# Kernel optimization log

Measured on AMD Instinct MI355X. Metric: run time of the kernel, lower is better.

Reference implementation:

```python
import jax, jax.numpy as jnp
import numpy as np

B, T, D, H = 2, 2048, 1024, 16
DH = D // H

def setup_inputs() -> dict:
    key = jax.random.key(0)
    ks = jax.random.split(key, 5)
    scale = 1.0 / np.sqrt(D)
    x = jax.random.normal(ks[0], (B, T, D), dtype=jnp.float32)
    Wq = jax.random.normal(ks[1], (D, D), dtype=jnp.float32) * scale
    Wk = jax.random.normal(ks[2], (D, D), dtype=jnp.float32) * scale
    Wv = jax.random.normal(ks[3], (D, D), dtype=jnp.float32) * scale
    Wo = jax.random.normal(ks[4], (D, D), dtype=jnp.float32) * scale
    # causal mask: True means masked (matches torch masked_fill semantics)
    mask = jnp.triu(jnp.ones((T, T), dtype=bool), k=1)
    return {"x": x, "mask": mask, "Wq": Wq, "Wk": Wk, "Wv": Wv, "Wo": Wo}

def reference(x, mask, Wq, Wk, Wv, Wo):
    b, t, c = x.shape
    # projections -> [B, H, T, DH]
    def split_heads(y):
        return y.reshape(b, t, H, DH).transpose(0, 2, 1, 3)
    q = split_heads(x @ Wq)
    k = split_heads(x @ Wk)
    v = split_heads(x @ Wv)
    # scores [B, H, T, T]
    att = jnp.einsum('bhqd,bhkd->bhqk', q, k) / jnp.sqrt(jnp.float32(DH))
    att = jnp.where(mask, -jnp.inf, att)
    att = jax.nn.softmax(att, axis=-1)
    # dropout=0.0 (eval-mode determinism)
    out = jnp.einsum('bhqk,bhkd->bhqd', att, v)
    out = out.transpose(0, 2, 1, 3).reshape(b, t, c)
    return out @ Wo
```

## Files before the change

kernel.cpp:

```cpp
#include <hip/hip_runtime.h>
#include <stdint.h>

typedef unsigned short u16;
typedef unsigned int u32;
typedef __attribute__((ext_vector_type(8))) short s16x8;
typedef __attribute__((ext_vector_type(4))) float f32x4;
typedef __attribute__((ext_vector_type(8))) unsigned short u16x8;
typedef __attribute__((ext_vector_type(4))) unsigned short u16x4;

#define T_ 2048
#define D_ 1024
#define H_ 16
#define DH_ 64

#define QSCALE_LOG2E 0.18033688011112042f

#if __has_builtin(__builtin_amdgcn_exp2f)
#define EXP2(x) __builtin_amdgcn_exp2f(x)
#else
#define EXP2(x) exp2f(x)
#endif

__device__ __forceinline__ float bf2f(u16 u) {
    union { unsigned int i; float f; } x; x.i = ((unsigned int)u) << 16; return x.f;
}
__device__ __forceinline__ u16 f2bf(float f) {
    union { float f; unsigned int i; } x; x.f = f;
    unsigned int u = x.i;
    u += 0x7fffu + ((u >> 16) & 1u);
    return (u16)(u >> 16);
}
__device__ __forceinline__ u32 pack_rn(float a, float b) {
    union { float f; u32 u; } ua, ub; ua.f = a; ub.f = b;
    return ((ua.u + 0x8000u) >> 16) | ((ub.u + 0x8000u) & 0xffff0000u);
}

__device__ __forceinline__ void gload16(const u16* g, u16* l) {
    __builtin_amdgcn_global_load_lds(
        (const __attribute__((address_space(1))) void*)g,
        (__attribute__((address_space(3))) void*)l,
        16, 0, 0);
}

__global__ __launch_bounds__(256) void cvt_x_kernel(const float* __restrict__ x,
                                                    u16* __restrict__ xb) {
    int i = (blockIdx.x * 256 + threadIdx.x) * 4;
    float4 v = *(const float4*)(x + i);
    u16x4 o;
    o[0] = f2bf(v.x); o[1] = f2bf(v.y); o[2] = f2bf(v.z); o[3] = f2bf(v.w);
    *(u16x4*)(xb + i) = o;
}

__global__ __launch_bounds__(256) void transpose_w_kernel(const float* __restrict__ Wq,
                                                          const float* __restrict__ Wk,
                                                          const float* __restrict__ Wv,
                                                          const float* __restrict__ Wo,
                                                          u16* __restrict__ WT) {
    __shared__ float tile[32][33];
    int s = blockIdx.z;
    const float* W = (s == 0) ? Wq : (s == 1) ? Wk : (s == 2) ? Wv : Wo;
    int n0 = blockIdx.x * 32;
    int k0 = blockIdx.y * 32;
    int tx = threadIdx.x, ty = threadIdx.y;
    #pragma unroll
    for (int j = 0; j < 32; j += 8)
        tile[ty + j][tx] = W[(k0 + ty + j) * D_ + n0 + tx];
    __syncthreads();
    u16* dst = WT + (size_t)s * D_ * D_;
    #pragma unroll
    for (int j = 0; j < 32; j += 8)
        dst[(n0 + ty + j) * D_ + k0 + tx] = f2bf(tile[tx][ty + j]);
}

template <int MODE>
__global__ __launch_bounds__(256) void gemm_bt(const u16* __restrict__ A,
                                               const u16* __restrict__ Bt,
                                               u16* __restrict__ Qw,
                                               u16* __restrict__ Kw,
                                               u16* __restrict__ Vw,
                                               float* __restrict__ Cout) {
    __shared__ __align__(16) u16 As[2][128 * 32];
    __shared__ __align__(16) u16 Bs[2][128 * 32];
    const int m0 = blockIdx.x * 128, n0 = blockIdx.y * 128;
    int tid = threadIdx.x;
    int w = tid >> 6, lane = tid & 63, quad = lane >> 4, l15 = lane & 15;
    int wr = w >> 1, wc = w & 1;

    int nb0 = (w << 7), nb1 = nb0 + 64;
    int c0 = nb0 + lane, c1 = nb1 + lane;
    int r0 = c0 >> 2, k0off = (c0 & 3) << 3;
    int r1 = c1 >> 2, k1off = (c1 & 3) << 3;
    const u16* Ar0 = A + (size_t)(m0 + r0) * D_ + k0off;
    const u16* Ar1 = A + (size_t)(m0 + r1) * D_ + k1off;
    const u16* Br0 = Bt + (size_t)(n0 + r0) * D_ + k0off;
    const u16* Br1 = Bt + (size_t)(n0 + r1) * D_ + k1off;

    f32x4 acc[4][4];
    #pragma unroll
    for (int mi = 0; mi < 4; ++mi)
        #pragma unroll
        for (int ni = 0; ni < 4; ++ni) acc[mi][ni] = (f32x4){0.f, 0.f, 0.f, 0.f};

    gload16(Ar0, &As[0][nb0 << 3]);
    gload16(Ar1, &As[0][nb1 << 3]);
    gload16(Br0, &Bs[0][nb0 << 3]);
    gload16(Br1, &Bs[0][nb1 << 3]);

    for (int k0 = 0; k0 < D_; k0 += 32) {
        int buf = (k0 >> 5) & 1;
        __syncthreads();
        if (k0 + 32 < D_) {
            int kn = k0 + 32;
            gload16(Ar0 + kn, &As[buf ^ 1][nb0 << 3]);
            gload16(Ar1 + kn, &As[buf ^ 1][nb1 << 3]);
            gload16(Br0 + kn, &Bs[buf ^ 1][nb0 << 3]);
            gload16(Br1 + kn, &Bs[buf ^ 1][nb1 << 3]);
        }
        s16x8 af[4], bf[4];
        #pragma unroll
        for (int mi = 0; mi < 4; ++mi)
            af[mi] = *(const s16x8*)&As[buf][((wr * 64 + mi * 16 + l15) << 5) + (quad << 3)];
        #pragma unroll
        for (int ni = 0; ni < 4; ++ni)
            bf[ni] = *(const s16x8*)&Bs[buf][((wc * 64 + ni * 16 + l15) << 5) + (quad << 3)];
        #pragma unroll
        for (int mi = 0; mi < 4; ++mi)
            #pragma unroll
            for (int ni = 0; ni < 4; ++ni)
                acc[mi][ni] = __builtin_amdgcn_mfma_f32_16x16x32_bf16(af[mi], bf[ni],
                                                                      acc[mi][ni], 0, 0, 0);
    }

    #pragma unroll
    for (int mi = 0; mi < 4; ++mi) {
        int mbase = m0 + wr * 64 + mi * 16 + quad * 4;
        #pragma unroll
        for (int ni = 0; ni < 4; ++ni) {
            int n = n0 + wc * 64 + ni * 16 + l15;
            if (MODE == 0) {
                int b = mbase >> 11, t0 = mbase & 2047;
                int sel = n >> 10, nn = n & 1023;
                int h = nn >> 6, dh = nn & 63;
                int bhidx = (b << 4) + h;
                if (sel == 0) {
                    #pragma unroll
                    for (int r = 0; r < 4; ++r)
                        Qw[(size_t)(bhidx * T_ + t0 + r) * DH_ + dh] =
                            f2bf(acc[mi][ni][r] * QSCALE_LOG2E);
                } else if (sel == 1) {
                    #pragma unroll
                    for (int r = 0; r < 4; ++r)
                        Kw[(size_t)(bhidx * T_ + t0 + r) * DH_ + dh] = f2bf(acc[mi][ni][r]);
                } else {
                    uint2 pk;
                    pk.x = pack_rn(acc[mi][ni][0], acc[mi][ni][1]);
                    pk.y = pack_rn(acc[mi][ni][2], acc[mi][ni][3]);
                    *(uint2*)(Vw + ((size_t)bhidx * DH_ + dh) * T_ + t0) = pk;
                }
            } else {
                #pragma unroll
                for (int r = 0; r < 4; ++r)
                    Cout[(size_t)(mbase + r) * D_ + n] = acc[mi][ni][r];
            }
        }
    }
}

__global__ __launch_bounds__(256) void attn_mfma_kernel(const u16* __restrict__ Qg,
                                                        const u16* __restrict__ Kg,
                                                        const u16* __restrict__ Vt,
                                                        u16* __restrict__ att) {
    __shared__ __align__(16) u16 Kbuf[2][64 * 64];
    __shared__ __align__(16) u16 Vbuf[2][64 * 64];
    __shared__ __align__(16) u16 Ps[4][16][72];

    int bx = (int)gridDim.x - 1 - (int)blockIdx.x;
    int bh = blockIdx.y;
    int tid = threadIdx.x;
    int w = tid >> 6, lane = tid & 63, quad = lane >> 4, l15 = lane & 15;
    int q0 = bx * 64;
    int q0w = q0 + 16 * w;

    const u16* Qb = Qg + (size_t)bh * T_ * DH_;
    const u16* Kb = Kg + (size_t)bh * T_ * DH_;
    const u16* Vb = Vt + (size_t)bh * DH_ * T_;

    s16x8 qb0 = *(const s16x8*)(Qb + (size_t)(q0w + l15) * DH_ + quad * 8);
    s16x8 qb1 = *(const s16x8*)(Qb + (size_t)(q0w + l15) * DH_ + quad * 8 + 32);

    int nb0 = (w << 7);
    int nb1 = (w << 7) + 64;
    int n0c = nb0 + lane, n1c = nb1 + lane;
    int r0 = n0c >> 3, c0s = n0c & 7, g0 = (r0 << 3) + (c0s ^ (r0 & 7));
    int r1 = n1c >> 3, c1s = n1c & 7, g1 = (r1 << 3) + (c1s ^ (r1 & 7));

    gload16(Kb + (g0 << 3), &Kbuf[0][nb0 << 3]);
    gload16(Kb + (g1 << 3), &Kbuf[0][nb1 << 3]);
    gload16(Vb + (size_t)r0 * T_ + ((g0 & 7) << 3), &Vbuf[0][nb0 << 3]);
    gload16(Vb + (size_t)r1 * T_ + ((g1 & 7) << 3), &Vbuf[0][nb1 << 3]);

    f32x4 og[4] = {{0.f,0.f,0.f,0.f},{0.f,0.f,0.f,0.f},{0.f,0.f,0.f,0.f},{0.f,0.f,0.f,0.f}};
    float lpart = 0.f;

    for (int kt = 0; kt <= bx; ++kt) {
        int buf = kt & 1;
        __syncthreads();

        if (kt < bx) {
            int kb2 = (kt + 1) << 6;
            const u16* Ktile = Kb + (size_t)kb2 * DH_;
            gload16(Ktile + (g0 << 3), &Kbuf[buf ^ 1][nb0 << 3]);
            gload16(Ktile + (g1 << 3), &Kbuf[buf ^ 1][nb1 << 3]);
            gload16(Vb + (size_t)r0 * T_ + kb2 + ((g0 & 7) << 3), &Vbuf[buf ^ 1][nb0 << 3]);
            gload16(Vb + (size_t)r1 * T_ + kb2 + ((g1 & 7) << 3), &Vbuf[buf ^ 1][nb1 << 3]);
        }

        f32x4 st[4];
        #pragma unroll
        for (int g = 0; g < 4; ++g) {
            int r = (g << 4) + l15;
            int cc = quad ^ (r & 7);
            s16x8 ka0 = *(const s16x8*)&Kbuf[buf][((r << 3) + cc) << 3];
            s16x8 ka1 = *(const s16x8*)&Kbuf[buf][((r << 3) + (cc ^ 4)) << 3];
            f32x4 z = {0.f, 0.f, 0.f, 0.f};
            st[g] = __builtin_amdgcn_mfma_f32_16x16x32_bf16(ka0, qb0, z, 0, 0, 0);
            st[g] = __builtin_amdgcn_mfma_f32_16x16x32_bf16(ka1, qb1, st[g], 0, 0, 0);
        }

        if (kt == bx) {
            int rowq = (w << 4) + l15;
            #pragma unroll
            for (int g = 0; g < 4; ++g)
                #pragma unroll
                for (int r = 0; r < 4; ++r)
                    if ((g << 4) + (quad << 2) + r > rowq) st[g][r] = -INFINITY;
        }

        #pragma unroll
        for (int g = 0; g < 4; ++g)
            #pragma unroll
            for (int r = 0; r < 4; ++r) {
                float p = EXP2(st[g][r]);
                st[g][r] = p;
                lpart += p;
            }

        #pragma unroll
        for (int g = 0; g < 4; ++g) {
            uint2 pk;
            pk.x = pack_rn(st[g][0], st[g][1]);
            pk.y = pack_rn(st[g][2], st[g][3]);
            *(uint2*)&Ps[w][l15][g * 16 + quad * 4] = pk;
        }
        s16x8 pb0 = *(const s16x8*)&Ps[w][l15][quad * 8];
        s16x8 pb1 = *(const s16x8*)&Ps[w][l15][quad * 8 + 32];

        #pragma unroll
        for (int g = 0; g < 4; ++g) {
            int r = (g << 4) + l15;
            int cc = quad ^ (r & 7);
            s16x8 va0 = *(const s16x8*)&Vbuf[buf][((r << 3) + cc) << 3];
            s16x8 va1 = *(const s16x8*)&Vbuf[buf][((r << 3) + (cc ^ 4)) << 3];
            og[g] = __builtin_amdgcn_mfma_f32_16x16x32_bf16(va0, pb0, og[g], 0, 0, 0);
            og[g] = __builtin_amdgcn_mfma_f32_16x16x32_bf16(va1, pb1, og[g], 0, 0, 0);
        }
    }

    float l = lpart;
    l += __shfl_xor(l, 16);
    l += __shfl_xor(l, 32);
    float inv = 1.f / l;
    int b = bh >> 4, h = bh & 15;
    u16* dst = att + (size_t)(b * T_ + q0w + l15) * D_ + (h << 6);
    #pragma unroll
    for (int g = 0; g < 4; ++g) {
        uint2 pk;
        pk.x = (u32)f2bf(og[g][0] * inv) | ((u32)f2bf(og[g][1] * inv) << 16);
        pk.y = (u32)f2bf(og[g][2] * inv) | ((u32)f2bf(og[g][3] * inv) << 16);
        *(uint2*)(dst + (g << 4) + (quad << 2)) = pk;
    }
}

extern "C" void kernel_launch(void* const* d_in, const int* in_sizes, int n_in,
                              void* d_out, int out_size, void* d_ws, size_t ws_size,
                              hipStream_t stream) {
    const float* x  = (const float*)d_in[0];
    const float* Wq = (const float*)d_in[2];
    const float* Wk = (const float*)d_in[3];
    const float* Wv = (const float*)d_in[4];
    const float* Wo = (const float*)d_in[5];
    float* out = (float*)d_out;

    char* ws = (char*)d_ws;
    u16* xb  = (u16*)(ws);
    u16* WT  = (u16*)(ws + (8ull  << 20));
    u16* Qw  = (u16*)(ws + (16ull << 20));
    u16* Kw  = (u16*)(ws + (24ull << 20));
    u16* Vw  = (u16*)(ws + (32ull << 20));
    u16* att = (u16*)(ws + (40ull << 20));

    cvt_x_kernel<<<dim3(4096), dim3(256), 0, stream>>>(x, xb);
    transpose_w_kernel<<<dim3(32, 32, 4), dim3(32, 8), 0, stream>>>(Wq, Wk, Wv, Wo, WT);
    gemm_bt<0><<<dim3(32, 24), dim3(256), 0, stream>>>(xb, WT, Qw, Kw, Vw, nullptr);
    attn_mfma_kernel<<<dim3(32, 32), dim3(256), 0, stream>>>(Qw, Kw, Vw, att);
    gemm_bt<1><<<dim3(32, 8), dim3(256), 0, stream>>>(att, WT + 3ull * 1048576ull,
                                                      nullptr, nullptr, nullptr, out);
}
```

Baseline: 215.0 us.

## Process 128 query rows per attention block and narrow output GEMM tiles

The attention kernel now has each block handle two 64-row query tiles, so every K/V tile staged in LDS feeds twice as many MFMAs, and the grid halves to 16x32. Causal masking is adjusted for the two sub-tiles. The output projection gets its own kernel with 128x64 tiles, doubling its block count from 256 to 512 to improve CU occupancy. The trade-offs are more registers per attention thread and fewer, longer attention blocks, which could worsen load balance across the causal triangle.

```diff
diff --git a/kernel.cpp b/kernel.cpp
--- a/kernel.cpp
+++ b/kernel.cpp
@@ -72,13 +72,11 @@
         dst[(n0 + ty + j) * D_ + k0 + tx] = f2bf(tile[tx][ty + j]);
 }
 
-template <int MODE>
-__global__ __launch_bounds__(256) void gemm_bt(const u16* __restrict__ A,
-                                               const u16* __restrict__ Bt,
-                                               u16* __restrict__ Qw,
-                                               u16* __restrict__ Kw,
-                                               u16* __restrict__ Vw,
-                                               float* __restrict__ Cout) {
+__global__ __launch_bounds__(256) void gemm_qkv(const u16* __restrict__ A,
+                                                const u16* __restrict__ Bt,
+                                                u16* __restrict__ Qw,
+                                                u16* __restrict__ Kw,
+                                                u16* __restrict__ Vw) {
     __shared__ __align__(16) u16 As[2][128 * 32];
     __shared__ __align__(16) u16 Bs[2][128 * 32];
     const int m0 = blockIdx.x * 128, n0 = blockIdx.y * 128;
@@ -137,31 +135,87 @@
         #pragma unroll
         for (int ni = 0; ni < 4; ++ni) {
             int n = n0 + wc * 64 + ni * 16 + l15;
-            if (MODE == 0) {
-                int b = mbase >> 11, t0 = mbase & 2047;
-                int sel = n >> 10, nn = n & 1023;
-                int h = nn >> 6, dh = nn & 63;
-                int bhidx = (b << 4) + h;
-                if (sel == 0) {
-                    #pragma unroll
-                    for (int r = 0; r < 4; ++r)
-                        Qw[(size_t)(bhidx * T_ + t0 + r) * DH_ + dh] =
-                            f2bf(acc[mi][ni][r] * QSCALE_LOG2E);
-                } else if (sel == 1) {
-                    #pragma unroll
-                    for (int r = 0; r < 4; ++r)
-                        Kw[(size_t)(bhidx * T_ + t0 + r) * DH_ + dh] = f2bf(acc[mi][ni][r]);
-                } else {
-                    uint2 pk;
-                    pk.x = pack_rn(acc[mi][ni][0], acc[mi][ni][1]);
-                    pk.y = pack_rn(acc[mi][ni][2], acc[mi][ni][3]);
-                    *(uint2*)(Vw + ((size_t)bhidx * DH_ + dh) * T_ + t0) = pk;
-                }
-            } else {
+            int b = mbase >> 11, t0 = mbase & 2047;
+            int sel = n >> 10, nn = n & 1023;
+            int h = nn >> 6, dh = nn & 63;
+            int bhidx = (b << 4) + h;
+            if (sel == 0) {
                 #pragma unroll
                 for (int r = 0; r < 4; ++r)
-                    Cout[(size_t)(mbase + r) * D_ + n] = acc[mi][ni][r];
+                    Qw[(size_t)(bhidx * T_ + t0 + r) * DH_ + dh] =
+                        f2bf(acc[mi][ni][r] * QSCALE_LOG2E);
+            } else if (sel == 1) {
+                #pragma unroll
+                for (int r = 0; r < 4; ++r)
+                    Kw[(size_t)(bhidx * T_ + t0 + r) * DH_ + dh] = f2bf(acc[mi][ni][r]);
+            } else {
+                uint2 pk;
+                pk.x = pack_rn(acc[mi][ni][0], acc[mi][ni][1]);
+                pk.y = pack_rn(acc[mi][ni][2], acc[mi][ni][3]);
+                *(uint2*)(Vw + ((size_t)bhidx * DH_ + dh) * T_ + t0) = pk;
             }
+        }
+    }
+}
+
+__global__ __launch_bounds__(256) void gemm_out(const u16* __restrict__ A,
+                                                const u16* __restrict__ Bt,
+                                                float* __restrict__ Cout) {
+    __shared__ __align__(16) u16 As[2][128 * 32];
+    __shared__ __align__(16) u16 Bs[2][64 * 32];
+    const int m0 = blockIdx.x * 128, n0 = blockIdx.y * 64;
+    int tid = threadIdx.x;
+    int w = tid >> 6, lane = tid & 63, quad = lane >> 4, l15 = lane & 15;
+
+    int nbA0 = (w << 7), nbA1 = nbA0 + 64, nbB = (w << 6);
+    int cA0 = nbA0 + lane, cA1 = nbA1 + lane, cB = nbB + lane;
+    const u16* ArA0 = A + (size_t)(m0 + (cA0 >> 2)) * D_ + ((cA0 & 3) << 3);
+    const u16* ArA1 = A + (size_t)(m0 + (cA1 >> 2)) * D_ + ((cA1 & 3) << 3);
+    const u16* BrB  = Bt + (size_t)(n0 + (cB >> 2)) * D_ + ((cB & 3) << 3);
+
+    f32x4 acc[2][4];
+    #pragma unroll
+    for (int mi = 0; mi < 2; ++mi)
+        #pragma unroll
+        for (int ni = 0; ni < 4; ++ni) acc[mi][ni] = (f32x4){0.f, 0.f, 0.f, 0.f};
+
+    gload16(ArA0, &As[0][nbA0 << 3]);
+    gload16(ArA1, &As[0][nbA1 << 3]);
+    gload16(BrB,  &Bs[0][nbB << 3]);
+
+    for (int k0 = 0; k0 < D_; k0 += 32) {
+        int buf = (k0 >> 5) & 1;
+        __syncthreads();
+        if (k0 + 32 < D_) {
+            int kn = k0 + 32;
+            gload16(ArA0 + kn, &As[buf ^ 1][nbA0 << 3]);
+            gload16(ArA1 + kn, &As[buf ^ 1][nbA1 << 3]);
+            gload16(BrB + kn,  &Bs[buf ^ 1][nbB << 3]);
+        }
+        s16x8 af[2], bf[4];
+        #pragma unroll
+        for (int mi = 0; mi < 2; ++mi)
+            af[mi] = *(const s16x8*)&As[buf][((w * 32 + mi * 16 + l15) << 5) + (quad << 3)];
+        #pragma unroll
+        for (int ni = 0; ni < 4; ++ni)
+            bf[ni] = *(const s16x8*)&Bs[buf][((ni * 16 + l15) << 5) + (quad << 3)];
+        #pragma unroll
+        for (int mi = 0; mi < 2; ++mi)
+            #pragma unroll
+            for (int ni = 0; ni < 4; ++ni)
+                acc[mi][ni] = __builtin_amdgcn_mfma_f32_16x16x32_bf16(af[mi], bf[ni],
+                                                                      acc[mi][ni], 0, 0, 0);
+    }
+
+    #pragma unroll
+    for (int mi = 0; mi < 2; ++mi) {
+        int mbase = m0 + w * 32 + mi * 16 + quad * 4;
+        #pragma unroll
+        for (int ni = 0; ni < 4; ++ni) {
+            int n = n0 + ni * 16 + l15;
+            #pragma unroll
+            for (int r = 0; r < 4; ++r)
+                Cout[(size_t)(mbase + r) * D_ + n] = acc[mi][ni][r];
         }
     }
 }
@@ -172,24 +226,26 @@
                                                         u16* __restrict__ att) {
     __shared__ __align__(16) u16 Kbuf[2][64 * 64];
     __shared__ __align__(16) u16 Vbuf[2][64 * 64];
-    __shared__ __align__(16) u16 Ps[4][16][72];
+    __shared__ __align__(16) u16 Ps[4][2][16][72];
 
     int bx = (int)gridDim.x - 1 - (int)blockIdx.x;
     int bh = blockIdx.y;
     int tid = threadIdx.x;
     int w = tid >> 6, lane = tid & 63, quad = lane >> 4, l15 = lane & 15;
-    int q0 = bx * 64;
-    int q0w = q0 + 16 * w;
+    int q0 = bx * 128;
+    int qA = q0 + 16 * w;
+    int qB = q0 + 64 + 16 * w;
 
     const u16* Qb = Qg + (size_t)bh * T_ * DH_;
     const u16* Kb = Kg + (size_t)bh * T_ * DH_;
     const u16* Vb = Vt + (size_t)bh * DH_ * T_;
 
-    s16x8 qb0 = *(const s16x8*)(Qb + (size_t)(q0w + l15) * DH_ + quad * 8);
-    s16x8 qb1 = *(const s16x8*)(Qb + (size_t)(q0w + l15) * DH_ + quad * 8 + 32);
-
-    int nb0 = (w << 7);
-    int nb1 = (w << 7) + 64;
+    s16x8 qa0 = *(const s16x8*)(Qb + (size_t)(qA + l15) * DH_ + quad * 8);
+    s16x8 qa1 = *(const s16x8*)(Qb + (size_t)(qA + l15) * DH_ + quad * 8 + 32);
+    s16x8 qc0 = *(const s16x8*)(Qb + (size_t)(qB + l15) * DH_ + quad * 8);
+    s16x8 qc1 = *(const s16x8*)(Qb + (size_t)(qB + l15) * DH_ + quad * 8 + 32);
+
+    int nb0 = (w << 7), nb1 = nb0 + 64;
     int n0c = nb0 + lane, n1c = nb1 + lane;
     int r0 = n0c >> 3, c0s = n0c & 7, g0 = (r0 << 3) + (c0s ^ (r0 & 7));
     int r1 = n1c >> 3, c1s = n1c & 7, g1 = (r1 << 3) + (c1s ^ (r1 & 7));
@@ -199,14 +255,16 @@
     gload16(Vb + (size_t)r0 * T_ + ((g0 & 7) << 3), &Vbuf[0][nb0 << 3]);
     gload16(Vb + (size_t)r1 * T_ + ((g1 & 7) << 3), &Vbuf[0][nb1 << 3]);
 
-    f32x4 og[4] = {{0.f,0.f,0.f,0.f},{0.f,0.f,0.f,0.f},{0.f,0.f,0.f,0.f},{0.f,0.f,0.f,0.f}};
-    float lpart = 0.f;
-
-    for (int kt = 0; kt <= bx; ++kt) {
+    f32x4 oA[4] = {{0.f,0.f,0.f,0.f},{0.f,0.f,0.f,0.f},{0.f,0.f,0.f,0.f},{0.f,0.f,0.f,0.f}};
+    f32x4 oB[4] = {{0.f,0.f,0.f,0.f},{0.f,0.f,0.f,0.f},{0.f,0.f,0.f,0.f},{0.f,0.f,0.f,0.f}};
+    float lA = 0.f, lB = 0.f;
+
+    int ktmax = 2 * bx + 1;
+    for (int kt = 0; kt <= ktmax; ++kt) {
         int buf = kt & 1;
         __syncthreads();
 
-        if (kt < bx) {
+        if (kt < ktmax) {
             int kb2 = (kt + 1) << 6;
             const u16* Ktile = Kb + (size_t)kb2 * DH_;
             gload16(Ktile + (g0 << 3), &Kbuf[buf ^ 1][nb0 << 3]);
@@ -215,7 +273,7 @@
             gload16(Vb + (size_t)r1 * T_ + kb2 + ((g1 & 7) << 3), &Vbuf[buf ^ 1][nb1 << 3]);
         }
 
-        f32x4 st[4];
+        f32x4 sA[4], sB[4];
         #pragma unroll
         for (int g = 0; g < 4; ++g) {
             int r = (g << 4) + l15;
@@ -223,37 +281,49 @@
             s16x8 ka0 = *(const s16x8*)&Kbuf[buf][((r << 3) + cc) << 3];
             s16x8 ka1 = *(const s16x8*)&Kbuf[buf][((r << 3) + (cc ^ 4)) << 3];
             f32x4 z = {0.f, 0.f, 0.f, 0.f};
-            st[g] = __builtin_amdgcn_mfma_f32_16x16x32_bf16(ka0, qb0, z, 0, 0, 0);
-            st[g] = __builtin_amdgcn_mfma_f32_16x16x32_bf16(ka1, qb1, st[g], 0, 0, 0);
-        }
-
-        if (kt == bx) {
-            int rowq = (w << 4) + l15;
+            sA[g] = __builtin_amdgcn_mfma_f32_16x16x32_bf16(ka0, qa0, z, 0, 0, 0);
+            sA[g] = __builtin_amdgcn_mfma_f32_16x16x32_bf16(ka1, qa1, sA[g], 0, 0, 0);
+            sB[g] = __builtin_amdgcn_mfma_f32_16x16x32_bf16(ka0, qc0, z, 0, 0, 0);
+            sB[g] = __builtin_amdgcn_mfma_f32_16x16x32_bf16(ka1, qc1, sB[g], 0, 0, 0);
+        }
+
+        if (kt >= ktmax - 1) {
+            int rA = q0 + 16 * w + l15 - (kt << 6);
             #pragma unroll
             for (int g = 0; g < 4; ++g)
                 #pragma unroll
                 for (int r = 0; r < 4; ++r)
-                    if ((g << 4) + (quad << 2) + r > rowq) st[g][r] = -INFINITY;
+                    if ((g << 4) + (quad << 2) + r > rA) sA[g][r] = -INFINITY;
+        }
+        if (kt == ktmax) {
+            int rB = 16 * w + l15;
+            #pragma unroll
+            for (int g = 0; g < 4; ++g)
+                #pragma unroll
+                for (int r = 0; r < 4; ++r)
+                    if ((g << 4) + (quad << 2) + r > rB) sB[g][r] = -INFINITY;
         }
 
         #pragma unroll
         for (int g = 0; g < 4; ++g)
             #pragma unroll
             for (int r = 0; r < 4; ++r) {
-                float p = EXP2(st[g][r]);
-                st[g][r] = p;
-                lpart += p;
+                float pA = EXP2(sA[g][r]); sA[g][r] = pA; lA += pA;
+                float pB = EXP2(sB[g][r]); sB[g][r] = pB; lB += pB;
             }
 
         #pragma unroll
         for (int g = 0; g < 4; ++g) {
-            uint2 pk;
-            pk.x = pack_rn(st[g][0], st[g][1]);
-            pk.y = pack_rn(st[g][2], st[g][3]);
-            *(uint2*)&Ps[w][l15][g * 16 + quad * 4] = pk;
-        }
-        s16x8 pb0 = *(const s16x8*)&Ps[w][l15][quad * 8];
-        s16x8 pb1 = *(const s16x8*)&Ps[w][l15][quad * 8 + 32];
+            uint2 pkA, pkB;
+            pkA.x = pack_rn(sA[g][0], sA[g][1]); pkA.y = pack_rn(sA[g][2], sA[g][3]);
+            pkB.x = pack_rn(sB[g][0], sB[g][1]); pkB.y = pack_rn(sB[g][2], sB[g][3]);
+            *(uint2*)&Ps[w][0][l15][g * 16 + quad * 4] = pkA;
+            *(uint2*)&Ps[w][1][l15][g * 16 + quad * 4] = pkB;
+        }
+        s16x8 pa0 = *(const s16x8*)&Ps[w][0][l15][quad * 8];
+        s16x8 pa1 = *(const s16x8*)&Ps[w][0][l15][quad * 8 + 32];
+        s16x8 pc0 = *(const s16x8*)&Ps[w][1][l15][quad * 8];
+        s16x8 pc1 = *(const s16x8*)&Ps[w][1][l15][quad * 8 + 32];
 
         #pragma unroll
         for (int g = 0; g < 4; ++g) {
@@ -261,23 +331,28 @@
             int cc = quad ^ (r & 7);
             s16x8 va0 = *(const s16x8*)&Vbuf[buf][((r << 3) + cc) << 3];
             s16x8 va1 = *(const s16x8*)&Vbuf[buf][((r << 3) + (cc ^ 4)) << 3];
-            og[g] = __builtin_amdgcn_mfma_f32_16x16x32_bf16(va0, pb0, og[g], 0, 0, 0);
-            og[g] = __builtin_amdgcn_mfma_f32_16x16x32_bf16(va1, pb1, og[g], 0, 0, 0);
-        }
-    }
-
-    float l = lpart;
-    l += __shfl_xor(l, 16);
-    l += __shfl_xor(l, 32);
-    float inv = 1.f / l;
+            oA[g] = __builtin_amdgcn_mfma_f32_16x16x32_bf16(va0, pa0, oA[g], 0, 0, 0);
+            oA[g] = __builtin_amdgcn_mfma_f32_16x16x32_bf16(va1, pa1, oA[g], 0, 0, 0);
+            oB[g] = __builtin_amdgcn_mfma_f32_16x16x32_bf16(va0, pc0, oB[g], 0, 0, 0);
+            oB[g] = __builtin_amdgcn_mfma_f32_16x16x32_bf16(va1, pc1, oB[g], 0, 0, 0);
+        }
+    }
+
+    lA += __shfl_xor(lA, 16); lA += __shfl_xor(lA, 32);
+    lB += __shfl_xor(lB, 16); lB += __shfl_xor(lB, 32);
+    float invA = 1.f / lA, invB = 1.f / lB;
     int b = bh >> 4, h = bh & 15;
-    u16* dst = att + (size_t)(b * T_ + q0w + l15) * D_ + (h << 6);
+    u16* dstA = att + (size_t)(b * T_ + qA + l15) * D_ + (h << 6);
+    u16* dstB = att + (size_t)(b * T_ + qB + l15) * D_ + (h << 6);
     #pragma unroll
     for (int g = 0; g < 4; ++g) {
         uint2 pk;
-        pk.x = (u32)f2bf(og[g][0] * inv) | ((u32)f2bf(og[g][1] * inv) << 16);
-        pk.y = (u32)f2bf(og[g][2] * inv) | ((u32)f2bf(og[g][3] * inv) << 16);
-        *(uint2*)(dst + (g << 4) + (quad << 2)) = pk;
+        pk.x = (u32)f2bf(oA[g][0] * invA) | ((u32)f2bf(oA[g][1] * invA) << 16);
+        pk.y = (u32)f2bf(oA[g][2] * invA) | ((u32)f2bf(oA[g][3] * invA) << 16);
+        *(uint2*)(dstA + (g << 4) + (quad << 2)) = pk;
+        pk.x = (u32)f2bf(oB[g][0] * invB) | ((u32)f2bf(oB[g][1] * invB) << 16);
+        pk.y = (u32)f2bf(oB[g][2] * invB) | ((u32)f2bf(oB[g][3] * invB) << 16);
+        *(uint2*)(dstB + (g << 4) + (quad << 2)) = pk;
     }
 }
 
@@ -301,8 +376,7 @@
 
     cvt_x_kernel<<<dim3(4096), dim3(256), 0, stream>>>(x, xb);
     transpose_w_kernel<<<dim3(32, 32, 4), dim3(32, 8), 0, stream>>>(Wq, Wk, Wv, Wo, WT);
-    gemm_bt<0><<<dim3(32, 24), dim3(256), 0, stream>>>(xb, WT, Qw, Kw, Vw, nullptr);
-    attn_mfma_kernel<<<dim3(32, 32), dim3(256), 0, stream>>>(Qw, Kw, Vw, att);
-    gemm_bt<1><<<dim3(32, 8), dim3(256), 0, stream>>>(att, WT + 3ull * 1048576ull,
-                                                      nullptr, nullptr, nullptr, out);
-}
+    gemm_qkv<<<dim3(32, 24), dim3(256), 0, stream>>>(xb, WT, Qw, Kw, Vw);
+    attn_mfma_kernel<<<dim3(16, 32), dim3(256), 0, stream>>>(Qw, Kw, Vw, att);
+    gemm_out<<<dim3(32, 16), dim3(256), 0, stream>>>(att, WT + 3ull * 1048576ull, out);
+}
```

New measurement: 209.4 us. 2.6% less time.
